# Kernel tuning notes

Measured on AMD Instinct MI355X. Metric: run time of the kernel, lower is better.

The kernel has to match this reference:

```python
import jax, jax.numpy as jnp
import numpy as np

HEADS = 16
DIM_HEAD = 64


def setup_inputs() -> dict:
    key = jax.random.key(0)
    k1, k2, k3, k4, k5 = jax.random.split(key, 5)
    B, S, E = 4, 2048, 1024
    inner = HEADS * DIM_HEAD  # 1024
    return {
        "hidden_states": jax.random.normal(k1, (B, S, E), dtype=jnp.float32),
        "w_q": jax.random.normal(k2, (E, inner), dtype=jnp.float32) * (E ** -0.5),
        "w_k": jax.random.normal(k3, (E, inner), dtype=jnp.float32) * (E ** -0.5),
        "w_v": jax.random.normal(k4, (E, inner), dtype=jnp.float32) * (E ** -0.5),
        "w_o": jax.random.normal(k5, (inner, E), dtype=jnp.float32) * (inner ** -0.5),
    }


def reference(hidden_states, w_q, w_k, w_v, w_o):
    # Self-attention path: context = hidden_states (context arg is None).
    B, S, _ = hidden_states.shape
    dtype = hidden_states.dtype
    scale = DIM_HEAD ** -0.5

    q = (hidden_states @ w_q).reshape(B, S, HEADS, DIM_HEAD)
    k = (hidden_states @ w_k).reshape(B, S, HEADS, DIM_HEAD)
    v = (hidden_states @ w_v).reshape(B, S, HEADS, DIM_HEAD)

    # fp32 softmax as in the original module
    q32 = q.astype(jnp.float32)
    k32 = k.astype(jnp.float32)
    scores = jnp.einsum('btnh,bfnh->bnft', k32, q32) * scale  # [B, H, S_q, S_kv]
    probs = jax.nn.softmax(scores, axis=-1).astype(dtype)

    out = jnp.einsum('bnft,btnh->bfnh', probs, v)  # [B, S, H, D]
    out = out.reshape(B, S, HEADS * DIM_HEAD)
    return out @ w_o  # [B, S, query_dim]
```

## Files before the change

### kernel.cpp

```cpp
#include <hip/hip_runtime.h>
#include <stdint.h>

typedef __attribute__((ext_vector_type(8))) unsigned short ushort8;
typedef __attribute__((ext_vector_type(8))) __bf16 bf16x8;
typedef __attribute__((ext_vector_type(4))) float f32x4;
typedef __attribute__((ext_vector_type(4))) uint32_t u32x4;

__device__ __forceinline__ unsigned short f2bf(float f) {
  union { float f; uint32_t u; } x; x.f = f;
  uint32_t u = x.u;
  uint32_t r = (u + 0x7fffu + ((u >> 16) & 1u)) >> 16;
  return (unsigned short)r;
}

__device__ __forceinline__ uint32_t pack_bf2(float lo, float hi) {
  return (uint32_t)f2bf(lo) | ((uint32_t)f2bf(hi) << 16);
}

__device__ __forceinline__ uint32_t rhu2(float lo, float hi) {
  union { float f; uint32_t u; } a, b; a.f = lo; b.f = hi;
  return __builtin_amdgcn_perm(b.u + 0x8000u, a.u + 0x8000u, 0x07060302u);
}

__device__ __forceinline__ void store_c(unsigned short* p, float v) { *p = f2bf(v); }
__device__ __forceinline__ void store_c(float* p, float v) { *p = v; }

__device__ __forceinline__ void gll16(const unsigned short* g, unsigned short* l) {
  __builtin_amdgcn_global_load_lds((const __attribute__((address_space(1))) void*)g,
                                   (__attribute__((address_space(3))) void*)l,
                                   16, 0, 0);
}

__global__ __launch_bounds__(256) void cvt_f32_bf16(
    const float* __restrict__ x, unsigned short* __restrict__ y, int n4) {
  int i = blockIdx.x * 256 + threadIdx.x;
  if (i >= n4) return;
  float4 v = *(const float4*)(x + (size_t)i * 4);
  uint2 p; p.x = pack_bf2(v.x, v.y); p.y = pack_bf2(v.z, v.w);
  *(uint2*)(y + (size_t)i * 4) = p;
}

__device__ __forceinline__ void transpose_body(const float* W, unsigned short* WT) {
  __shared__ unsigned short tile[32][33];
  int c0 = blockIdx.x * 32, r0 = blockIdx.y * 32;
  int x = threadIdx.x, y = threadIdx.y;
#pragma unroll
  for (int i = 0; i < 32; i += 8)
    tile[y + i][x] = f2bf(W[(size_t)(r0 + y + i) * 1024 + c0 + x]);
  __syncthreads();
#pragma unroll
  for (int i = 0; i < 32; i += 8)
    WT[(size_t)(c0 + y + i) * 1024 + r0 + x] = tile[x][y + i];
}

__global__ void transpose_w(const float* __restrict__ W,
                            unsigned short* __restrict__ WT) {
  transpose_body(W, WT);
}

__global__ void transpose_w3(const float* W0, const float* W1, const float* W2,
                             unsigned short* T0, unsigned short* T1,
                             unsigned short* T2) {
  const float* W = (blockIdx.z == 0) ? W0 : (blockIdx.z == 1) ? W1 : W2;
  unsigned short* WT = (blockIdx.z == 0) ? T0 : (blockIdx.z == 1) ? T1 : T2;
  transpose_body(W, WT);
}

template <typename OutT>
__global__ __launch_bounds__(256, 2) void gemm3(
    const unsigned short* A,
    const unsigned short* BT0, const unsigned short* BT1, const unsigned short* BT2,
    OutT* C0, OutT* C1, OutT* C2,
    int M, int N, int K, float sc0) {
  const unsigned short* BT = (blockIdx.z == 0) ? BT0 : (blockIdx.z == 1) ? BT1 : BT2;
  OutT* C = (blockIdx.z == 0) ? C0 : (blockIdx.z == 1) ? C1 : C2;
  const float sc = (blockIdx.z == 0) ? sc0 : 1.0f;

  __shared__ __attribute__((aligned(16))) unsigned short As[2][128 * 64];
  __shared__ __attribute__((aligned(16))) unsigned short Bs[2][128 * 64];

  const int tid = threadIdx.x;
  const int wave = tid >> 6, lane = tid & 63;
  const int fr = lane & 15, fq = lane >> 4;
  const int wm = wave >> 1, wn = wave & 1;
  const int bm = blockIdx.x * 128, bn = blockIdx.y * 128;

  const int r8 = tid >> 3, c8 = tid & 7;
  const int s8 = c8 ^ (r8 & 7);
  const unsigned short* Ag = A + (size_t)(bm + r8) * K + s8 * 8;
  const unsigned short* Bg = BT + (size_t)(bn + r8) * K + s8 * 8;

  f32x4 acc[4][4] = {};
  const int rx = fr & 7;

  const int NT = K >> 6;

#pragma unroll
  for (int i = 0; i < 4; i++) {
    gll16(Ag + (size_t)(i * 32) * K, &As[0][(i * 32 + wave * 8) * 64]);
    gll16(Bg + (size_t)(i * 32) * K, &Bs[0][(i * 32 + wave * 8) * 64]);
  }

  int cur = 0;
  for (int t = 0; t < NT; ++t) {
    __syncthreads();

    if (t + 1 < NT) {
      const int b = cur ^ 1;
      const size_t k0 = (size_t)(t + 1) * 64;
#pragma unroll
      for (int i = 0; i < 4; i++) {
        gll16(Ag + k0 + (size_t)(i * 32) * K, &As[b][(i * 32 + wave * 8) * 64]);
        gll16(Bg + k0 + (size_t)(i * 32) * K, &Bs[b][(i * 32 + wave * 8) * 64]);
      }
    }

#pragma unroll
    for (int kh = 0; kh < 2; ++kh) {
      bf16x8 af[4], bfr[4];
#pragma unroll
      for (int mt = 0; mt < 4; mt++)
        af[mt] = *(const bf16x8*)&As[cur][(wm * 64 + mt * 16 + fr) * 64 +
                                          (((kh * 4 + fq) ^ rx) * 8)];
#pragma unroll
      for (int nt = 0; nt < 4; nt++)
        bfr[nt] = *(const bf16x8*)&Bs[cur][(wn * 64 + nt * 16 + fr) * 64 +
                                           (((kh * 4 + fq) ^ rx) * 8)];
#pragma unroll
      for (int mt = 0; mt < 4; mt++)
#pragma unroll
        for (int nt = 0; nt < 4; nt++)
          acc[mt][nt] = __builtin_amdgcn_mfma_f32_16x16x32_bf16(af[mt], bfr[nt], acc[mt][nt], 0, 0, 0);
    }
    cur ^= 1;
  }

#pragma unroll
  for (int mt = 0; mt < 4; mt++)
#pragma unroll
    for (int nt = 0; nt < 4; nt++)
#pragma unroll
      for (int r = 0; r < 4; r++) {
        int row = bm + wm * 64 + mt * 16 + fq * 4 + r;
        int col = bn + wn * 64 + nt * 16 + fr;
        store_c(&C[(size_t)row * N + col], acc[mt][nt][r] * sc);
      }
}

__global__ __launch_bounds__(256, 4) void attn_kernel(
    const unsigned short* q, const unsigned short* k,
    const unsigned short* v, unsigned short* o) {
  const int S = 2048, E = 1024;
  __shared__ __attribute__((aligned(16))) unsigned short Ksb[2 * 64 * 64];
  __shared__ __attribute__((aligned(16))) unsigned short Vtb[64 * 64];

  const int tid = threadIdx.x;
  const int wave = tid >> 6, lane = tid & 63;
  const int fr = lane & 15, fq = lane >> 4;
  const int q0 = blockIdx.x * 128;
  const int bh = blockIdx.y;
  const int b = bh >> 4, h = bh & 15;
  const size_t base = ((size_t)b * S) * E + (size_t)h * 64;

  bf16x8 aq[2][2];
#pragma unroll
  for (int qg = 0; qg < 2; qg++)
#pragma unroll
    for (int ks = 0; ks < 2; ks++)
      aq[qg][ks] = *(const bf16x8*)&q[base +
          (size_t)(q0 + qg * 64 + wave * 16 + fr) * E + ks * 32 + fq * 8];

  ushort8 ones_u;
#pragma unroll
  for (int j = 0; j < 8; j++) ones_u[j] = 0x3F80;
  bf16x8 onesf = *(bf16x8*)&ones_u;

  f32x4 ot[2][4] = {};
  f32x4 osum[2] = {};

  const int srow = lane >> 3;
  const int scol = (((lane & 7) ^ srow) << 3);
  const unsigned short* Kg = k + base + (size_t)(wave * 16 + srow) * E + scol;

  const int rp = (tid & 31) * 2;
  const int dcv = (tid >> 5) * 8;
  const int u_ = rp & 31;
  const int slot = 32 * (rp >> 5) + 8 * ((u_ & 15) >> 2) + 4 * (u_ >> 4) + (u_ & 3);
  const unsigned short* Vg = v + base + (size_t)rp * E + dcv;

  const int rx = (fr & 7) << 3;

  gll16(Kg, &Ksb[wave * 1024]);
  gll16(Kg + 8 * (size_t)E, &Ksb[wave * 1024 + 512]);
  u32x4 va = *(const u32x4*)(Vg);
  u32x4 vb = *(const u32x4*)(Vg + E);

  int cur = 0;
  for (int t = 0; t < 32; t++) {
    const int nxt = cur ^ 4096;

    __syncthreads();

#pragma unroll
    for (int w = 0; w < 4; w++) {
      uint32_t lo = __builtin_amdgcn_perm(vb[w], va[w], 0x05040100u);
      uint32_t hi = __builtin_amdgcn_perm(vb[w], va[w], 0x07060302u);
      int d = dcv + 2 * w;
      *(uint32_t*)&Vtb[d * 64 + (slot ^ ((2 * w) << 3))] = lo;
      *(uint32_t*)&Vtb[(d + 1) * 64 + (slot ^ ((2 * w + 1) << 3))] = hi;
    }

    f32x4 st[2][4] = {};
    __builtin_amdgcn_s_setprio(1);
#pragma unroll
    for (int ks = 0; ks < 2; ks++) {
#pragma unroll
      for (int tt = 0; tt < 4; tt++) {
        bf16x8 ak = *(const bf16x8*)&Ksb[cur + (tt * 16 + fr) * 64 +
                                         ((ks * 32 + fq * 8) ^ rx)];
        st[0][tt] = __builtin_amdgcn_mfma_f32_16x16x32_bf16(ak, aq[0][ks], st[0][tt], 0, 0, 0);
        st[1][tt] = __builtin_amdgcn_mfma_f32_16x16x32_bf16(ak, aq[1][ks], st[1][tt], 0, 0, 0);
      }
    }
    __builtin_amdgcn_s_setprio(0);

    __syncthreads();

    if (t < 31) {
      const size_t poff = (size_t)(t + 1) * 64 * E;
      gll16(Kg + poff, &Ksb[nxt + wave * 1024]);
      gll16(Kg + poff + 8 * (size_t)E, &Ksb[nxt + wave * 1024 + 512]);
      va = *(const u32x4*)(Vg + poff);
      vb = *(const u32x4*)(Vg + poff + E);
    }

    uint32_t pk[2][4][2];
#pragma unroll
    for (int qg = 0; qg < 2; qg++)
#pragma unroll
      for (int tt = 0; tt < 4; tt++) {
        float e0 = __builtin_amdgcn_exp2f(st[qg][tt][0]);
        float e1 = __builtin_amdgcn_exp2f(st[qg][tt][1]);
        float e2 = __builtin_amdgcn_exp2f(st[qg][tt][2]);
        float e3 = __builtin_amdgcn_exp2f(st[qg][tt][3]);
        pk[qg][tt][0] = rhu2(e0, e1);
        pk[qg][tt][1] = rhu2(e2, e3);
      }

    __builtin_amdgcn_s_setprio(1);
#pragma unroll
    for (int c = 0; c < 2; c++) {
      bf16x8 bp[2];
#pragma unroll
      for (int qg = 0; qg < 2; qg++) {
        u32x4 bpr;
        bpr[0] = pk[qg][2 * c][0];
        bpr[1] = pk[qg][2 * c][1];
        bpr[2] = pk[qg][2 * c + 1][0];
        bpr[3] = pk[qg][2 * c + 1][1];
        bp[qg] = *(bf16x8*)&bpr;
      }
#pragma unroll
      for (int dt = 0; dt < 4; dt++) {
        bf16x8 av = *(const bf16x8*)&Vtb[(dt * 16 + fr) * 64 +
                                         ((c * 32 + fq * 8) ^ rx)];
        ot[0][dt] = __builtin_amdgcn_mfma_f32_16x16x32_bf16(av, bp[0], ot[0][dt], 0, 0, 0);
        ot[1][dt] = __builtin_amdgcn_mfma_f32_16x16x32_bf16(av, bp[1], ot[1][dt], 0, 0, 0);
      }
      osum[0] = __builtin_amdgcn_mfma_f32_16x16x32_bf16(onesf, bp[0], osum[0], 0, 0, 0);
      osum[1] = __builtin_amdgcn_mfma_f32_16x16x32_bf16(onesf, bp[1], osum[1], 0, 0, 0);
    }
    __builtin_amdgcn_s_setprio(0);

    cur = nxt;
  }

#pragma unroll
  for (int qg = 0; qg < 2; qg++) {
    float inv = 1.0f / osum[qg][0];
    size_t rowbase = base + (size_t)(q0 + qg * 64 + wave * 16 + fr) * E;
#pragma unroll
    for (int dt = 0; dt < 4; dt++) {
      uint32_t w0 = rhu2(ot[qg][dt][0] * inv, ot[qg][dt][1] * inv);
      uint32_t w1 = rhu2(ot[qg][dt][2] * inv, ot[qg][dt][3] * inv);
      *(uint32_t*)&o[rowbase + dt * 16 + fq * 4] = w0;
      *(uint32_t*)&o[rowbase + dt * 16 + fq * 4 + 2] = w1;
    }
  }
}

extern "C" void kernel_launch(void* const* d_in, const int* in_sizes, int n_in,
                              void* d_out, int out_size, void* d_ws, size_t ws_size,
                              hipStream_t stream) {
  const float* hs = (const float*)d_in[0];
  const float* wq = (const float*)d_in[1];
  const float* wk = (const float*)d_in[2];
  const float* wv = (const float*)d_in[3];
  const float* wo = (const float*)d_in[4];
  unsigned short* ws = (unsigned short*)d_ws;

  unsigned short* wqT = ws;
  unsigned short* wkT = ws + 1048576;
  unsigned short* wvT = ws + 2097152;
  unsigned short* woT = wqT;
  unsigned short* qb  = ws + 3145728;
  unsigned short* kb  = qb + 8388608;
  unsigned short* vb  = kb + 8388608;
  unsigned short* ob  = qb;
  unsigned short* hsb = (unsigned short*)d_out;
  float* out = (float*)d_out;

  const int M = 8192, N = 1024, K = 1024;
  const float KSC = 0.125f * 1.44269504088896341f;

  cvt_f32_bf16<<<dim3(M * K / 4 / 256), 256, 0, stream>>>(hs, hsb, M * K / 4);

  dim3 tb(32, 8);
  transpose_w3<<<dim3(32, 32, 3), tb, 0, stream>>>(wq, wk, wv, wqT, wkT, wvT);

  gemm3<unsigned short><<<dim3(M / 128, N / 128, 3), 256, 0, stream>>>(
      hsb, wqT, wkT, wvT, qb, kb, vb, M, N, K, KSC);

  transpose_w<<<dim3(32, 32), tb, 0, stream>>>(wo, woT);

  attn_kernel<<<dim3(2048 / 128, 64), 256, 0, stream>>>(qb, kb, vb, ob);

  gemm3<float><<<dim3(M / 128, N / 128, 1), 256, 0, stream>>>(
      ob, woT, woT, woT, out, out, out, M, N, K, 1.0f);
}
```

Baseline: 260.9 us.

## Fuse fp32-to-bf16 hidden-state conversion into QKV GEMM A-tile load

Removes the separate conversion kernel and instead loads fp32 hidden states directly in the QKV GEMM, converting to bf16 in registers and writing the swizzled tile into LDS between the two k-halves of compute. This drops a full write and re-read of the bf16 activation copy. The cost is that the fp32 A operand is read three times (once per Q/K/V grid slice) at twice the bytes, and loads go through registers instead of direct global-to-LDS. The attention kernel also switches its exp/pack of probabilities to native __bf16 casts, which changes rounding from round-half-up to round-to-nearest-even.

```diff
diff --git a/kernel.cpp b/kernel.cpp
--- a/kernel.cpp
+++ b/kernel.cpp
@@ -13,10 +13,6 @@
   return (unsigned short)r;
 }
 
-__device__ __forceinline__ uint32_t pack_bf2(float lo, float hi) {
-  return (uint32_t)f2bf(lo) | ((uint32_t)f2bf(hi) << 16);
-}
-
 __device__ __forceinline__ uint32_t rhu2(float lo, float hi) {
   union { float f; uint32_t u; } a, b; a.f = lo; b.f = hi;
   return __builtin_amdgcn_perm(b.u + 0x8000u, a.u + 0x8000u, 0x07060302u);
@@ -29,15 +25,6 @@
   __builtin_amdgcn_global_load_lds((const __attribute__((address_space(1))) void*)g,
                                    (__attribute__((address_space(3))) void*)l,
                                    16, 0, 0);
-}
-
-__global__ __launch_bounds__(256) void cvt_f32_bf16(
-    const float* __restrict__ x, unsigned short* __restrict__ y, int n4) {
-  int i = blockIdx.x * 256 + threadIdx.x;
-  if (i >= n4) return;
-  float4 v = *(const float4*)(x + (size_t)i * 4);
-  uint2 p; p.x = pack_bf2(v.x, v.y); p.y = pack_bf2(v.z, v.w);
-  *(uint2*)(y + (size_t)i * 4) = p;
 }
 
 __device__ __forceinline__ void transpose_body(const float* W, unsigned short* WT) {
@@ -66,9 +53,9 @@
   transpose_body(W, WT);
 }
 
-template <typename OutT>
+template <typename OutT, bool AF32>
 __global__ __launch_bounds__(256, 2) void gemm3(
-    const unsigned short* A,
+    const unsigned short* A16, const float* A32,
     const unsigned short* BT0, const unsigned short* BT1, const unsigned short* BT2,
     OutT* C0, OutT* C1, OutT* C2,
     int M, int N, int K, float sc0) {
@@ -87,7 +74,10 @@
 
   const int r8 = tid >> 3, c8 = tid & 7;
   const int s8 = c8 ^ (r8 & 7);
-  const unsigned short* Ag = A + (size_t)(bm + r8) * K + s8 * 8;
+  const unsigned short* Ag = nullptr;
+  const float* Ag32 = nullptr;
+  if constexpr (AF32) Ag32 = A32 + (size_t)(bm + r8) * K + c8 * 8;
+  else                Ag   = A16 + (size_t)(bm + r8) * K + s8 * 8;
   const unsigned short* Bg = BT + (size_t)(bn + r8) * K + s8 * 8;
 
   f32x4 acc[4][4] = {};
@@ -95,28 +85,54 @@
 
   const int NT = K >> 6;
 
-#pragma unroll
-  for (int i = 0; i < 4; i++) {
-    gll16(Ag + (size_t)(i * 32) * K, &As[0][(i * 32 + wave * 8) * 64]);
+  auto cvt8 = [](float4 a0, float4 a1) {
+    bf16x8 w;
+    w[0] = (__bf16)a0.x; w[1] = (__bf16)a0.y; w[2] = (__bf16)a0.z; w[3] = (__bf16)a0.w;
+    w[4] = (__bf16)a1.x; w[5] = (__bf16)a1.y; w[6] = (__bf16)a1.z; w[7] = (__bf16)a1.w;
+    return w;
+  };
+
+  if constexpr (AF32) {
+#pragma unroll
+    for (int i = 0; i < 4; i++) {
+      float4 a0 = *(const float4*)(Ag32 + (size_t)(i * 32) * K);
+      float4 a1 = *(const float4*)(Ag32 + (size_t)(i * 32) * K + 4);
+      *(bf16x8*)&As[0][(i * 32 + r8) * 64 + s8 * 8] = cvt8(a0, a1);
+    }
+  } else {
+#pragma unroll
+    for (int i = 0; i < 4; i++)
+      gll16(Ag + (size_t)(i * 32) * K, &As[0][(i * 32 + wave * 8) * 64]);
+  }
+#pragma unroll
+  for (int i = 0; i < 4; i++)
     gll16(Bg + (size_t)(i * 32) * K, &Bs[0][(i * 32 + wave * 8) * 64]);
-  }
 
   int cur = 0;
   for (int t = 0; t < NT; ++t) {
     __syncthreads();
 
+    const int b = cur ^ 1;
+    float4 fa0[4], fa1[4];
     if (t + 1 < NT) {
-      const int b = cur ^ 1;
       const size_t k0 = (size_t)(t + 1) * 64;
-#pragma unroll
-      for (int i = 0; i < 4; i++) {
-        gll16(Ag + k0 + (size_t)(i * 32) * K, &As[b][(i * 32 + wave * 8) * 64]);
+      if constexpr (AF32) {
+#pragma unroll
+        for (int i = 0; i < 4; i++) {
+          fa0[i] = *(const float4*)(Ag32 + k0 + (size_t)(i * 32) * K);
+          fa1[i] = *(const float4*)(Ag32 + k0 + (size_t)(i * 32) * K + 4);
+        }
+      } else {
+#pragma unroll
+        for (int i = 0; i < 4; i++)
+          gll16(Ag + k0 + (size_t)(i * 32) * K, &As[b][(i * 32 + wave * 8) * 64]);
+      }
+#pragma unroll
+      for (int i = 0; i < 4; i++)
         gll16(Bg + k0 + (size_t)(i * 32) * K, &Bs[b][(i * 32 + wave * 8) * 64]);
-      }
-    }
-
-#pragma unroll
-    for (int kh = 0; kh < 2; ++kh) {
+    }
+
+    auto compute = [&](int kh) {
       bf16x8 af[4], bfr[4];
 #pragma unroll
       for (int mt = 0; mt < 4; mt++)
@@ -131,7 +147,16 @@
 #pragma unroll
         for (int nt = 0; nt < 4; nt++)
           acc[mt][nt] = __builtin_amdgcn_mfma_f32_16x16x32_bf16(af[mt], bfr[nt], acc[mt][nt], 0, 0, 0);
-    }
+    };
+
+    compute(0);
+    if (AF32 && t + 1 < NT) {
+#pragma unroll
+      for (int i = 0; i < 4; i++)
+        *(bf16x8*)&As[b][(i * 32 + r8) * 64 + s8 * 8] = cvt8(fa0[i], fa1[i]);
+    }
+    compute(1);
+
     cur ^= 1;
   }
 
@@ -234,41 +259,30 @@
       vb = *(const u32x4*)(Vg + poff + E);
     }
 
-    uint32_t pk[2][4][2];
-#pragma unroll
-    for (int qg = 0; qg < 2; qg++)
-#pragma unroll
-      for (int tt = 0; tt < 4; tt++) {
-        float e0 = __builtin_amdgcn_exp2f(st[qg][tt][0]);
-        float e1 = __builtin_amdgcn_exp2f(st[qg][tt][1]);
-        float e2 = __builtin_amdgcn_exp2f(st[qg][tt][2]);
-        float e3 = __builtin_amdgcn_exp2f(st[qg][tt][3]);
-        pk[qg][tt][0] = rhu2(e0, e1);
-        pk[qg][tt][1] = rhu2(e2, e3);
+    bf16x8 bp[2][2];
+#pragma unroll
+    for (int c = 0; c < 2; c++)
+#pragma unroll
+      for (int qg = 0; qg < 2; qg++) {
+        bf16x8 vv;
+#pragma unroll
+        for (int j = 0; j < 8; j++)
+          vv[j] = (__bf16)__builtin_amdgcn_exp2f(st[qg][2 * c + (j >> 2)][j & 3]);
+        bp[c][qg] = vv;
       }
 
     __builtin_amdgcn_s_setprio(1);
 #pragma unroll
     for (int c = 0; c < 2; c++) {
-      bf16x8 bp[2];
-#pragma unroll
-      for (int qg = 0; qg < 2; qg++) {
-        u32x4 bpr;
-        bpr[0] = pk[qg][2 * c][0];
-        bpr[1] = pk[qg][2 * c][1];
-        bpr[2] = pk[qg][2 * c + 1][0];
-        bpr[3] = pk[qg][2 * c + 1][1];
-        bp[qg] = *(bf16x8*)&bpr;
-      }
 #pragma unroll
       for (int dt = 0; dt < 4; dt++) {
         bf16x8 av = *(const bf16x8*)&Vtb[(dt * 16 + fr) * 64 +
                                          ((c * 32 + fq * 8) ^ rx)];
-        ot[0][dt] = __builtin_amdgcn_mfma_f32_16x16x32_bf16(av, bp[0], ot[0][dt], 0, 0, 0);
-        ot[1][dt] = __builtin_amdgcn_mfma_f32_16x16x32_bf16(av, bp[1], ot[1][dt], 0, 0, 0);
-      }
-      osum[0] = __builtin_amdgcn_mfma_f32_16x16x32_bf16(onesf, bp[0], osum[0], 0, 0, 0);
-      osum[1] = __builtin_amdgcn_mfma_f32_16x16x32_bf16(onesf, bp[1], osum[1], 0, 0, 0);
+        ot[0][dt] = __builtin_amdgcn_mfma_f32_16x16x32_bf16(av, bp[c][0], ot[0][dt], 0, 0, 0);
+        ot[1][dt] = __builtin_amdgcn_mfma_f32_16x16x32_bf16(av, bp[c][1], ot[1][dt], 0, 0, 0);
+      }
+      osum[0] = __builtin_amdgcn_mfma_f32_16x16x32_bf16(onesf, bp[c][0], osum[0], 0, 0, 0);
+      osum[1] = __builtin_amdgcn_mfma_f32_16x16x32_bf16(onesf, bp[c][1], osum[1], 0, 0, 0);
     }
     __builtin_amdgcn_s_setprio(0);
 
@@ -307,24 +321,21 @@
   unsigned short* kb  = qb + 8388608;
   unsigned short* vb  = kb + 8388608;
   unsigned short* ob  = qb;
-  unsigned short* hsb = (unsigned short*)d_out;
   float* out = (float*)d_out;
 
   const int M = 8192, N = 1024, K = 1024;
   const float KSC = 0.125f * 1.44269504088896341f;
 
-  cvt_f32_bf16<<<dim3(M * K / 4 / 256), 256, 0, stream>>>(hs, hsb, M * K / 4);
-
   dim3 tb(32, 8);
   transpose_w3<<<dim3(32, 32, 3), tb, 0, stream>>>(wq, wk, wv, wqT, wkT, wvT);
 
-  gemm3<unsigned short><<<dim3(M / 128, N / 128, 3), 256, 0, stream>>>(
-      hsb, wqT, wkT, wvT, qb, kb, vb, M, N, K, KSC);
+  gemm3<unsigned short, true><<<dim3(M / 128, N / 128, 3), 256, 0, stream>>>(
+      nullptr, hs, wqT, wkT, wvT, qb, kb, vb, M, N, K, KSC);
 
   transpose_w<<<dim3(32, 32), tb, 0, stream>>>(wo, woT);
 
   attn_kernel<<<dim3(2048 / 128, 64), 256, 0, stream>>>(qb, kb, vb, ob);
 
-  gemm3<float><<<dim3(M / 128, N / 128, 1), 256, 0, stream>>>(
-      ob, woT, woT, woT, out, out, out, M, N, K, 1.0f);
-}
+  gemm3<float, false><<<dim3(M / 128, N / 128, 1), 256, 0, stream>>>(
+      ob, nullptr, woT, woT, woT, out, out, out, M, N, K, 1.0f);
+}
```

New measurement: 278.7 us. +6.8%, slower.
